# Optimization experiments

Measured on AMD Instinct MI355X. Metric: run time of the kernel, lower is better.

The kernel has to match this reference:

```python
import jax, jax.numpy as jnp
import numpy as np

EMBED = 1024
FF = 4096
HEADS = 16
HEAD_SIZE = EMBED // HEADS


def setup_inputs() -> dict:
    key = jax.random.key(0)
    ks = jax.random.split(key, 12)
    s = 0.02
    inp = {
        "x": jax.random.normal(ks[0], (2, 2048, EMBED), dtype=jnp.float32),
        "Wq": jax.random.normal(ks[1], (EMBED, EMBED), dtype=jnp.float32) * s,
        "bq": jnp.zeros((EMBED,), jnp.float32),
        "Wk": jax.random.normal(ks[2], (EMBED, EMBED), dtype=jnp.float32) * s,
        "bk": jnp.zeros((EMBED,), jnp.float32),
        "Wv": jax.random.normal(ks[3], (EMBED, EMBED), dtype=jnp.float32) * s,
        "bv": jnp.zeros((EMBED,), jnp.float32),
        "Wo": jax.random.normal(ks[4], (EMBED, EMBED), dtype=jnp.float32) * s,
        "bo": jnp.zeros((EMBED,), jnp.float32),
        "W1": jax.random.normal(ks[5], (EMBED, FF), dtype=jnp.float32) * s,
        "b1": jnp.zeros((FF,), jnp.float32),
        "W2": jax.random.normal(ks[6], (FF, EMBED), dtype=jnp.float32) * s,
        "b2": jnp.zeros((EMBED,), jnp.float32),
        "ln1_g": jnp.ones((EMBED,), jnp.float32),
        "ln1_b": jnp.zeros((EMBED,), jnp.float32),
        "ln2_g": jnp.ones((EMBED,), jnp.float32),
        "ln2_b": jnp.zeros((EMBED,), jnp.float32),
    }
    return inp


def _layernorm(x, g, b, eps=1e-5):
    mu = jnp.mean(x, axis=-1, keepdims=True)
    var = jnp.var(x, axis=-1, keepdims=True)
    return (x - mu) * jax.lax.rsqrt(var + eps) * g + b


def _attn(x, Wq, bq, Wk, bk, Wv, bv, Wo, bo):
    B, S, E = x.shape
    q = (x @ Wq + bq).reshape(B, S, HEADS, HEAD_SIZE)
    k = (x @ Wk + bk).reshape(B, S, HEADS, HEAD_SIZE)
    v = (x @ Wv + bv).reshape(B, S, HEADS, HEAD_SIZE)
    # full (non-causal) attention, scores materialized as in the original
    att = jnp.einsum('bqhd,bkhd->bhqk', q, k) / jnp.sqrt(jnp.float32(HEAD_SIZE))
    att = jax.nn.softmax(att, axis=-1)
    out = jnp.einsum('bhqk,bkhd->bqhd', att, v).reshape(B, S, E)
    return out @ Wo + bo


def reference(x, Wq, bq, Wk, bk, Wv, bv, Wo, bo, W1, b1, W2, b2,
              ln1_g, ln1_b, ln2_g, ln2_b):
    x = x + _attn(_layernorm(x, ln1_g, ln1_b), Wq, bq, Wk, bk, Wv, bv, Wo, bo)
    h = _layernorm(x, ln2_g, ln2_b)
    x = x + (jax.nn.gelu(h @ W1 + b1) @ W2 + b2)
    return x
```

## Files before the change

kernel.cpp:

```cpp
#include <hip/hip_runtime.h>

typedef __bf16 bf16;
typedef __bf16 bf16x8 __attribute__((ext_vector_type(8)));
typedef __bf16 bf16x4 __attribute__((ext_vector_type(4)));
typedef float f32x4 __attribute__((ext_vector_type(4)));

#define EMBED 1024
#define FFDIM 4096
#define HEADS 16
#define HD 64
#define SEQ 2048
#define BATCH 2
#define TOKENS (BATCH * SEQ)
#define MB (1u << 20)


__device__ __forceinline__ void gld16(const void* g, void* l) {
  __builtin_amdgcn_global_load_lds(
      (const __attribute__((address_space(1))) void*)g,
      (__attribute__((address_space(3))) void*)l, 16, 0, 0);
}

__device__ __forceinline__ float gelu_f(float x) {
  float u = 0.7978845608028654f * (x + 0.044715f * x * x * x);
  float t = tanhf(u);
  return 0.5f * x * (1.0f + t);
}

__device__ __forceinline__ void xcd_tiles(int nx, int& tx, int& ty) {
  int lid = blockIdx.x + nx * blockIdx.y;
  tx = (lid >> 3) % nx;
  ty = ((lid / (8 * nx)) << 3) | (lid & 7);
}

__global__ __launch_bounds__(256) void transpose_cast(const float* __restrict__ in,
                                                      bf16* __restrict__ out,
                                                      int R, int C) {
  __shared__ float t[32][33];
  int bx = blockIdx.x * 32;
  int by = blockIdx.y * 32;
  int tx = threadIdx.x & 31;
  int ty = threadIdx.x >> 5;
#pragma unroll
  for (int i = 0; i < 32; i += 8)
    t[ty + i][tx] = in[(size_t)(by + ty + i) * C + bx + tx];
  __syncthreads();
#pragma unroll
  for (int i = 0; i < 32; i += 8)
    out[(size_t)(bx + ty + i) * R + by + tx] = (bf16)t[tx][ty + i];
}

__global__ __launch_bounds__(256) void ln_kernel(const float* __restrict__ x,
                                                 const float* __restrict__ g,
                                                 const float* __restrict__ b,
                                                 bf16* __restrict__ out) {
  int tok = blockIdx.x;
  int tid = threadIdx.x;
  const float4* xv = (const float4*)(x + (size_t)tok * EMBED);
  float4 v = xv[tid];
  float s = v.x + v.y + v.z + v.w;
  float s2 = v.x * v.x + v.y * v.y + v.z * v.z + v.w * v.w;
#pragma unroll
  for (int off = 32; off >= 1; off >>= 1) {
    s += __shfl_xor(s, off, 64);
    s2 += __shfl_xor(s2, off, 64);
  }
  __shared__ float ps[4], ps2[4];
  int w = tid >> 6;
  if ((tid & 63) == 0) { ps[w] = s; ps2[w] = s2; }
  __syncthreads();
  s = ps[0] + ps[1] + ps[2] + ps[3];
  s2 = ps2[0] + ps2[1] + ps2[2] + ps2[3];
  float mu = s * (1.0f / EMBED);
  float var = s2 * (1.0f / EMBED) - mu * mu;
  float r = rsqrtf(var + 1e-5f);
  float4 gg = ((const float4*)g)[tid];
  float4 bb = ((const float4*)b)[tid];
  bf16x4 o;
  o[0] = (bf16)((v.x - mu) * r * gg.x + bb.x);
  o[1] = (bf16)((v.y - mu) * r * gg.y + bb.y);
  o[2] = (bf16)((v.z - mu) * r * gg.z + bb.z);
  o[3] = (bf16)((v.w - mu) * r * gg.w + bb.w);
  ((bf16x4*)(out + (size_t)tok * EMBED))[tid] = o;
}

template <int MODE>
__global__ __launch_bounds__(256) void gemm_bt(const bf16* __restrict__ A,
                                               const bf16* __restrict__ BT,
                                               const float* __restrict__ bias,
                                               void* __restrict__ out,
                                               int M, int N, int K,
                                               const float* __restrict__ bias2,
                                               const float* __restrict__ bias3,
                                               void* __restrict__ out2,
                                               void* __restrict__ out3) {
  __shared__ bf16 ldsA[128 * 32];
  __shared__ bf16 ldsB[128 * 32];
  int tid = threadIdx.x;
  int wave = tid >> 6, lane = tid & 63;
  int lquad = lane >> 4, l15 = lane & 15;
  int wm = wave >> 1, wn = wave & 1;
  int txs, tys;
  xcd_tiles(N >> 7, txs, tys);
  int tileM = tys * 128, tileN = txs * 128;

  f32x4 acc[4][4];
#pragma unroll
  for (int i = 0; i < 4; i++)
#pragma unroll
    for (int j = 0; j < 4; j++) acc[i][j] = (f32x4){0.f, 0.f, 0.f, 0.f};

  int srow = lane >> 2;
  int schunk = (lane & 3) * 8;

  for (int k0 = 0; k0 < K; k0 += 32) {
    __syncthreads();
#pragma unroll
    for (int c = 0; c < 2; c++) {
      int rowA = tileM + wave * 32 + c * 16 + srow;
      gld16(&A[(size_t)rowA * K + k0 + schunk], &ldsA[(wave * 32 + c * 16) * 32]);
      int rowB = tileN + wave * 32 + c * 16 + srow;
      gld16(&BT[(size_t)rowB * K + k0 + schunk], &ldsB[(wave * 32 + c * 16) * 32]);
    }
    __syncthreads();

    bf16x8 aF[4], bF[4];
#pragma unroll
    for (int i = 0; i < 4; i++)
      aF[i] = *(const bf16x8*)&ldsA[(wm * 64 + i * 16 + l15) * 32 + lquad * 8];
#pragma unroll
    for (int j = 0; j < 4; j++)
      bF[j] = *(const bf16x8*)&ldsB[(wn * 64 + j * 16 + l15) * 32 + lquad * 8];
#pragma unroll
    for (int i = 0; i < 4; i++)
#pragma unroll
      for (int j = 0; j < 4; j++)
        acc[i][j] = __builtin_amdgcn_mfma_f32_16x16x32_bf16(aF[i], bF[j], acc[i][j], 0, 0, 0);
  }

  int r0 = tileM + wm * 64;
  int c0 = tileN + wn * 64;
#pragma unroll
  for (int i = 0; i < 4; i++) {
#pragma unroll
    for (int j = 0; j < 4; j++) {
      int col = c0 + j * 16 + l15;
      float bv;
      if (MODE == 4) {
        int sel = col >> 10, cc = col & 1023;
        bv = (sel == 0 ? bias : sel == 1 ? bias2 : bias3)[cc];
      } else {
        bv = bias[col];
      }
#pragma unroll
      for (int r = 0; r < 4; r++) {
        int row = r0 + i * 16 + lquad * 4 + r;
        float v = acc[i][j][r] + bv;
        if (MODE == 0) {
          ((bf16*)out)[(size_t)row * N + col] = (bf16)v;
        } else if (MODE == 3) {
          ((bf16*)out)[(size_t)row * N + col] = (bf16)gelu_f(v);
        } else {
          int sel = col >> 10, cc = col & 1023;
          if (sel == 0) {
            ((bf16*)out)[(size_t)row * EMBED + cc] = (bf16)v;
          } else if (sel == 1) {
            ((bf16*)out2)[(size_t)row * EMBED + cc] = (bf16)v;
          } else {
            int bb = row >> 11, s = row & (SEQ - 1);
            ((bf16*)out3)[((size_t)(bb * EMBED + cc)) * SEQ + s] = (bf16)v;
          }
        }
      }
    }
  }
}

__global__ __launch_bounds__(256) void gemm_bt64(const bf16* __restrict__ A,
                                                 const bf16* __restrict__ BT,
                                                 const float* __restrict__ bias,
                                                 const float* __restrict__ res,
                                                 float* __restrict__ out,
                                                 int M, int N, int K) {
  __shared__ bf16 ldsA[128 * 64];
  __shared__ bf16 ldsB[64 * 64];
  int tid = threadIdx.x;
  int wave = tid >> 6, lane = tid & 63;
  int lquad = lane >> 4, l15 = lane & 15;
  int wm = wave >> 1, wn = wave & 1;
  int txs, tys;
  xcd_tiles(N >> 6, txs, tys);
  int tileM = tys * 128, tileN = txs * 64;

  f32x4 acc[4][2];
#pragma unroll
  for (int i = 0; i < 4; i++)
#pragma unroll
    for (int j = 0; j < 2; j++) acc[i][j] = (f32x4){0.f, 0.f, 0.f, 0.f};

  int srow = lane >> 3;
  int sch = lane & 7;

  for (int k0 = 0; k0 < K; k0 += 64) {
    __syncthreads();
#pragma unroll
    for (int c = 0; c < 4; c++) {
      int base = wave * 32 + c * 8;
      int row = base + srow;
      int ch = sch ^ (row & 7);
      gld16(&A[(size_t)(tileM + row) * K + k0 + ch * 8], &ldsA[base * 64]);
    }
#pragma unroll
    for (int c = 0; c < 2; c++) {
      int base = wave * 16 + c * 8;
      int row = base + srow;
      int ch = sch ^ (row & 7);
      gld16(&BT[(size_t)(tileN + row) * K + k0 + ch * 8], &ldsB[base * 64]);
    }
    __syncthreads();

    bf16x8 aF[2][4], bF[2][2];
#pragma unroll
    for (int ks = 0; ks < 2; ks++) {
#pragma unroll
      for (int i = 0; i < 4; i++) {
        int R = wm * 64 + i * 16 + l15;
        int ch = (ks * 4 + lquad) ^ (R & 7);
        aF[ks][i] = *(const bf16x8*)&ldsA[R * 64 + ch * 8];
      }
#pragma unroll
      for (int j = 0; j < 2; j++) {
        int R = wn * 32 + j * 16 + l15;
        int ch = (ks * 4 + lquad) ^ (R & 7);
        bF[ks][j] = *(const bf16x8*)&ldsB[R * 64 + ch * 8];
      }
    }
#pragma unroll
    for (int i = 0; i < 4; i++)
#pragma unroll
      for (int j = 0; j < 2; j++)
#pragma unroll
        for (int ks = 0; ks < 2; ks++)
          acc[i][j] = __builtin_amdgcn_mfma_f32_16x16x32_bf16(aF[ks][i], bF[ks][j], acc[i][j], 0, 0, 0);
  }

  int r0 = tileM + wm * 64;
  int c0 = tileN + wn * 32;
#pragma unroll
  for (int i = 0; i < 4; i++) {
#pragma unroll
    for (int j = 0; j < 2; j++) {
      int col = c0 + j * 16 + l15;
      float bv = bias[col];
#pragma unroll
      for (int r = 0; r < 4; r++) {
        int row = r0 + i * 16 + lquad * 4 + r;
        out[(size_t)row * N + col] = acc[i][j][r] + bv + res[(size_t)row * N + col];
      }
    }
  }
}

__global__ __launch_bounds__(256) void attn_kernel(const bf16* __restrict__ q,
                                                   const bf16* __restrict__ k,
                                                   const bf16* __restrict__ vT,
                                                   bf16* __restrict__ o) {
  int lid = blockIdx.x;
  int qb = (lid >> 3) & 31;
  int g = (lid & 7) | ((lid >> 8) << 3);
  int h = g & 15, b = g >> 4;
  int tid = threadIdx.x;
  int w = tid >> 6, lane = tid & 63;
  int lquad = lane >> 4, l15 = lane & 15;

  __shared__ bf16 ldsK[128 * 64];
  __shared__ bf16 ldsV[64 * 128];
  __shared__ bf16 ldsP[4][16 * 136];

  int qrow = b * SEQ + qb * 64 + w * 16 + l15;
  bf16x8 qB[2];
  qB[0] = *(const bf16x8*)&q[(size_t)qrow * EMBED + h * HD + 0 + lquad * 8];
  qB[1] = *(const bf16x8*)&q[(size_t)qrow * EMBED + h * HD + 32 + lquad * 8];

  f32x4 O[4];
#pragma unroll
  for (int j = 0; j < 4; j++) O[j] = (f32x4){0.f, 0.f, 0.f, 0.f};
  float m = -1e30f, lsum = 0.f;
  const float C2 = 0.18033688011112042f;

  for (int kb = 0; kb < SEQ; kb += 128) {
    __syncthreads();
#pragma unroll
    for (int c = 0; c < 4; c++) {
      int base = w * 32 + c * 8;
      int row = base + (lane >> 3);
      int ch = (lane & 7) ^ (row & 7);
      gld16(&k[(size_t)(b * SEQ + kb + row) * EMBED + h * HD + ch * 8],
            &ldsK[base * 64]);
    }
#pragma unroll
    for (int c = 0; c < 4; c++) {
      int base = w * 16 + c * 4;
      int row = base + (lane >> 4);
      int ch = (lane & 15) ^ (row & 7);
      gld16(&vT[(size_t)(b * EMBED + h * HD + row) * SEQ + kb + ch * 8],
            &ldsV[base * 128]);
    }
    __syncthreads();

    f32x4 st[8];
#pragma unroll
    for (int t = 0; t < 8; t++) {
      st[t] = (f32x4){0.f, 0.f, 0.f, 0.f};
#pragma unroll
      for (int ks = 0; ks < 2; ks++) {
        int R = t * 16 + l15;
        int ch = (ks * 4 + lquad) ^ (R & 7);
        bf16x8 kA = *(const bf16x8*)&ldsK[R * 64 + ch * 8];
        st[t] = __builtin_amdgcn_mfma_f32_16x16x32_bf16(kA, qB[ks], st[t], 0, 0, 0);
      }
    }

    float mt = fmaxf(fmaxf(st[0][0], st[0][1]), fmaxf(st[0][2], st[0][3]));
#pragma unroll
    for (int t = 1; t < 8; t++) {
      float a0 = fmaxf(st[t][0], st[t][1]);
      float a1 = fmaxf(st[t][2], st[t][3]);
      mt = fmaxf(mt, fmaxf(a0, a1));
    }
    mt = fmaxf(mt, __shfl_xor(mt, 16, 64));
    mt = fmaxf(mt, __shfl_xor(mt, 32, 64));
    float mn = fmaxf(m, mt);
    float alpha = __builtin_amdgcn_exp2f((m - mn) * C2);
    m = mn;
    float mc2 = m * C2;

    float rs = 0.f;
#pragma unroll
    for (int t = 0; t < 8; t++)
#pragma unroll
      for (int r = 0; r < 4; r++) {
        st[t][r] = __builtin_amdgcn_exp2f(fmaf(st[t][r], C2, -mc2));
        rs += st[t][r];
      }
    lsum = lsum * alpha + rs;
#pragma unroll
    for (int j = 0; j < 4; j++)
#pragma unroll
      for (int r = 0; r < 4; r++) O[j][r] *= alpha;

#pragma unroll
    for (int t = 0; t < 8; t++) {
      bf16x4 pk;
#pragma unroll
      for (int r = 0; r < 4; r++) pk[r] = (bf16)st[t][r];
      *(bf16x4*)&ldsP[w][l15 * 136 + t * 16 + lquad * 4] = pk;
    }
    bf16x8 pB[4];
#pragma unroll
    for (int ks2 = 0; ks2 < 4; ks2++)
      pB[ks2] = *(const bf16x8*)&ldsP[w][l15 * 136 + ks2 * 32 + lquad * 8];

#pragma unroll
    for (int j = 0; j < 4; j++) {
#pragma unroll
      for (int ks2 = 0; ks2 < 4; ks2++) {
        int R = j * 16 + l15;
        int ch = (ks2 * 4 + lquad) ^ (R & 7);
        bf16x8 vA = *(const bf16x8*)&ldsV[R * 128 + ch * 8];
        O[j] = __builtin_amdgcn_mfma_f32_16x16x32_bf16(vA, pB[ks2], O[j], 0, 0, 0);
      }
    }
  }

  lsum += __shfl_xor(lsum, 16, 64);
  lsum += __shfl_xor(lsum, 32, 64);
  float inv = 1.0f / lsum;
  int tok = b * SEQ + qb * 64 + w * 16 + l15;
#pragma unroll
  for (int j = 0; j < 4; j++) {
    bf16x4 ov;
#pragma unroll
    for (int r = 0; r < 4; r++) ov[r] = (bf16)(O[j][r] * inv);
    *(bf16x4*)&o[(size_t)tok * EMBED + h * HD + j * 16 + lquad * 4] = ov;
  }
}


extern "C" void kernel_launch(void* const* d_in, const int* in_sizes, int n_in,
                              void* d_out, int out_size, void* d_ws, size_t ws_size,
                              hipStream_t stream) {
  const float* x = (const float*)d_in[0];
  const float* Wq = (const float*)d_in[1];
  const float* bq = (const float*)d_in[2];
  const float* Wk = (const float*)d_in[3];
  const float* bk = (const float*)d_in[4];
  const float* Wv = (const float*)d_in[5];
  const float* bv = (const float*)d_in[6];
  const float* Wo = (const float*)d_in[7];
  const float* bo = (const float*)d_in[8];
  const float* W1 = (const float*)d_in[9];
  const float* b1 = (const float*)d_in[10];
  const float* W2 = (const float*)d_in[11];
  const float* b2 = (const float*)d_in[12];
  const float* ln1_g = (const float*)d_in[13];
  const float* ln1_b = (const float*)d_in[14];
  const float* ln2_g = (const float*)d_in[15];
  const float* ln2_b = (const float*)d_in[16];

  char* ws = (char*)d_ws;
  bf16* WqT = (bf16*)(ws + 0 * MB);
  bf16* WkT = (bf16*)(ws + 2 * MB);
  bf16* WvT = (bf16*)(ws + 4 * MB);
  bf16* WoT = (bf16*)(ws + 6 * MB);
  bf16* W1T = (bf16*)(ws + 8 * MB);
  bf16* W2T = (bf16*)(ws + 16 * MB);
  bf16* xn1 = (bf16*)(ws + 24 * MB);
  bf16* qbuf = (bf16*)(ws + 32 * MB);
  bf16* kbuf = (bf16*)(ws + 40 * MB);
  bf16* vT = (bf16*)(ws + 48 * MB);
  bf16* attnb = (bf16*)(ws + 56 * MB);
  float* x2f = (float*)(ws + 64 * MB);
  bf16* xn2 = (bf16*)(ws + 80 * MB);
  bf16* hb = (bf16*)(ws + 88 * MB);
  float* outf = (float*)d_out;

  transpose_cast<<<dim3(32, 32), 256, 0, stream>>>(Wq, WqT, EMBED, EMBED);
  transpose_cast<<<dim3(32, 32), 256, 0, stream>>>(Wk, WkT, EMBED, EMBED);
  transpose_cast<<<dim3(32, 32), 256, 0, stream>>>(Wv, WvT, EMBED, EMBED);
  transpose_cast<<<dim3(32, 32), 256, 0, stream>>>(Wo, WoT, EMBED, EMBED);
  transpose_cast<<<dim3(128, 32), 256, 0, stream>>>(W1, W1T, EMBED, FFDIM);
  transpose_cast<<<dim3(32, 128), 256, 0, stream>>>(W2, W2T, FFDIM, EMBED);

  ln_kernel<<<TOKENS, 256, 0, stream>>>(x, ln1_g, ln1_b, xn1);

  gemm_bt<4><<<dim3(3072 / 128, TOKENS / 128), 256, 0, stream>>>(
      xn1, WqT, bq, qbuf, TOKENS, 3072, EMBED, bk, bv, kbuf, vT);

  attn_kernel<<<dim3(SEQ / 64 * HEADS * BATCH), 256, 0, stream>>>(qbuf, kbuf, vT, attnb);

  gemm_bt64<<<dim3(EMBED / 64, TOKENS / 128), 256, 0, stream>>>(
      attnb, WoT, bo, x, x2f, TOKENS, EMBED, EMBED);

  ln_kernel<<<TOKENS, 256, 0, stream>>>(x2f, ln2_g, ln2_b, xn2);

  gemm_bt<3><<<dim3(FFDIM / 128, TOKENS / 128), 256, 0, stream>>>(
      xn2, W1T, b1, hb, TOKENS, FFDIM, EMBED,
      nullptr, nullptr, nullptr, nullptr);
  gemm_bt64<<<dim3(EMBED / 64, TOKENS / 128), 256, 0, stream>>>(
      hb, W2T, b2, x2f, outf, TOKENS, EMBED, FFDIM);
}
```

Before: 412.5 us.

## Deepen GEMM K-tile to 64 with XOR-swizzled LDS and drop XCD tile remap

The GEMM main loop now stages 64-wide K slices instead of 32, which halves the number of barrier pairs per tile and doubles the MFMA work done between them. The LDS layout is XOR-swizzled by row so that fragment reads from the 128-byte rows avoid bank conflicts. The XCD-aware tile remapping is replaced with plain blockIdx mapping, which may reduce L2 locality across chiplets. LDS use per block doubles, which could lower occupancy.

```diff
diff --git a/kernel.cpp b/kernel.cpp
--- a/kernel.cpp
+++ b/kernel.cpp
@@ -94,15 +94,13 @@
                                                const float* __restrict__ bias3,
                                                void* __restrict__ out2,
                                                void* __restrict__ out3) {
-  __shared__ bf16 ldsA[128 * 32];
-  __shared__ bf16 ldsB[128 * 32];
+  __shared__ bf16 ldsA[128 * 64];
+  __shared__ bf16 ldsB[128 * 64];
   int tid = threadIdx.x;
   int wave = tid >> 6, lane = tid & 63;
   int lquad = lane >> 4, l15 = lane & 15;
   int wm = wave >> 1, wn = wave & 1;
-  int txs, tys;
-  xcd_tiles(N >> 7, txs, tys);
-  int tileM = tys * 128, tileN = txs * 128;
+  int tileM = blockIdx.y * 128, tileN = blockIdx.x * 128;
 
   f32x4 acc[4][4];
 #pragma unroll
@@ -110,32 +108,44 @@
 #pragma unroll
     for (int j = 0; j < 4; j++) acc[i][j] = (f32x4){0.f, 0.f, 0.f, 0.f};
 
-  int srow = lane >> 2;
-  int schunk = (lane & 3) * 8;
-
-  for (int k0 = 0; k0 < K; k0 += 32) {
-    __syncthreads();
-#pragma unroll
-    for (int c = 0; c < 2; c++) {
-      int rowA = tileM + wave * 32 + c * 16 + srow;
-      gld16(&A[(size_t)rowA * K + k0 + schunk], &ldsA[(wave * 32 + c * 16) * 32]);
-      int rowB = tileN + wave * 32 + c * 16 + srow;
-      gld16(&BT[(size_t)rowB * K + k0 + schunk], &ldsB[(wave * 32 + c * 16) * 32]);
-    }
-    __syncthreads();
-
-    bf16x8 aF[4], bF[4];
+  int srow = lane >> 3;
+  int sch = lane & 7;
+
+  for (int k0 = 0; k0 < K; k0 += 64) {
+    __syncthreads();
+#pragma unroll
+    for (int c = 0; c < 4; c++) {
+      int base = wave * 32 + c * 8;
+      int row = base + srow;
+      int ch = sch ^ (row & 7);
+      gld16(&A[(size_t)(tileM + row) * K + k0 + ch * 8], &ldsA[base * 64]);
+      gld16(&BT[(size_t)(tileN + row) * K + k0 + ch * 8], &ldsB[base * 64]);
+    }
+    __syncthreads();
+
+    bf16x8 aF[2][4], bF[2][4];
+#pragma unroll
+    for (int ks = 0; ks < 2; ks++) {
+#pragma unroll
+      for (int i = 0; i < 4; i++) {
+        int R = wm * 64 + i * 16 + l15;
+        int ch = (ks * 4 + lquad) ^ (R & 7);
+        aF[ks][i] = *(const bf16x8*)&ldsA[R * 64 + ch * 8];
+      }
+#pragma unroll
+      for (int j = 0; j < 4; j++) {
+        int R = wn * 64 + j * 16 + l15;
+        int ch = (ks * 4 + lquad) ^ (R & 7);
+        bF[ks][j] = *(const bf16x8*)&ldsB[R * 64 + ch * 8];
+      }
+    }
 #pragma unroll
     for (int i = 0; i < 4; i++)
-      aF[i] = *(const bf16x8*)&ldsA[(wm * 64 + i * 16 + l15) * 32 + lquad * 8];
-#pragma unroll
-    for (int j = 0; j < 4; j++)
-      bF[j] = *(const bf16x8*)&ldsB[(wn * 64 + j * 16 + l15) * 32 + lquad * 8];
-#pragma unroll
-    for (int i = 0; i < 4; i++)
 #pragma unroll
       for (int j = 0; j < 4; j++)
-        acc[i][j] = __builtin_amdgcn_mfma_f32_16x16x32_bf16(aF[i], bF[j], acc[i][j], 0, 0, 0);
+#pragma unroll
+        for (int ks = 0; ks < 2; ks++)
+          acc[i][j] = __builtin_amdgcn_mfma_f32_16x16x32_bf16(aF[ks][i], bF[ks][j], acc[i][j], 0, 0, 0);
   }
 
   int r0 = tileM + wm * 64;
```

Measured after the change: 401.1 us. -2.8%, faster.
